# Kernel optimization log

Hardware: AMD Instinct MI355X
Metric: run time of the kernel (lower is better)

## Reference

```python
import jax, jax.numpy as jnp
import numpy as np

N_ATOMS = 262144          # 2**18 atoms
N_PAIRS = 16777216        # 2**24 pairs (~64 neighbors/atom)
SIGMA = 1.0
EPSILON = 1.0
CUTOFF = 2.5              # 2.5 * sigma (module default)


def setup_inputs() -> dict:
    key = jax.random.key(0)
    k_pos, k_i, k_off = jax.random.split(key, 3)
    # Gaussian cloud, scale 2 -> typical pair distances O(1-5), many inside cutoff
    positions = 2.0 * jax.random.normal(k_pos, (N_ATOMS, 3), dtype=jnp.float32)
    # Large box; shifts are zero so cell does not alter displacements
    cell = 100.0 * jnp.eye(3, dtype=jnp.float32)
    # Neighbor-list style pairs; guarantee j != i so distances are strictly > 0
    i = jax.random.randint(k_i, (N_PAIRS,), 0, N_ATOMS, dtype=jnp.int32)
    off = jax.random.randint(k_off, (N_PAIRS,), 1, N_ATOMS, dtype=jnp.int32)
    j = (i + off) % N_ATOMS
    mapping = jnp.stack([i, j])  # [2, n_pairs]
    shifts = jnp.zeros((N_PAIRS, 3), dtype=jnp.float32)
    return {"positions": positions, "cell": cell, "mapping": mapping, "shifts": shifts}


def reference(positions, cell, mapping, shifts):
    # Gather pair displacements: dr = r_j - r_i + shifts @ cell (row-vector cell)
    i, j = mapping[0], mapping[1]
    dr_vec = positions[j] - positions[i] + shifts @ cell      # [P, 3]
    distances = jnp.sqrt(jnp.sum(dr_vec * dr_vec, axis=-1))   # [P]

    # Lennard-Jones 12-6 pair energy: 4 eps ((s/r)^12 - (s/r)^6)
    sr6 = (SIGMA / distances) ** 6
    sr12 = sr6 * sr6
    pair_energies = 4.0 * EPSILON * (sr12 - sr6)
    mask = distances < CUTOFF
    pair_energies = jnp.where(mask, pair_energies, 0.0)
    energy = 0.5 * jnp.sum(pair_energies)

    # Pair force magnitude: 24 eps / r * (2 (s/r)^12 - (s/r)^6)
    pair_forces = 24.0 * EPSILON / distances * (2.0 * sr12 - sr6)
    pair_forces = jnp.where(mask, pair_forces, 0.0)
    force_vectors = (pair_forces / distances)[:, None] * dr_vec  # [P, 3]

    # Scatter-add back to atoms: -fv at i, +fv at j
    forces = (jnp.zeros_like(positions)
              .at[i].add(-force_vectors)
              .at[j].add(force_vectors))
    return energy, forces
```

## Files before the change

kernel.cpp:

```cpp
#include <hip/hip_runtime.h>

#define N_ATOMS 262144
#define N_PAIRS 16777216
#define FCOMP (N_ATOMS * 3)

#define NB      256
#define BSHIFT  10
#define ALOCAL  (N_ATOMS / NB)
#define CAPBB   32
#define SC_THREADS 256
#define NPT     32
#define PPB     (SC_THREADS * NPT)
#define G_TOTAL (N_PAIRS / PPB)
#define ACC_THREADS 1024

typedef int          v4i __attribute__((ext_vector_type(4)));
typedef float        v4f __attribute__((ext_vector_type(4)));
typedef unsigned int u32;
typedef u32          v4u __attribute__((ext_vector_type(4)));


__device__ __forceinline__ void atomic_add_f32(float* addr, float v) {
    unsafeAtomicAdd(addr, v);
}
__device__ __forceinline__ float scrub_nonfinite(float x) {
    return ((__float_as_uint(x) & 0x7f800000u) == 0x7f800000u) ? 0.0f : x;
}

__global__ void __launch_bounds__(256) lj_prep_kernel(
    const float* __restrict__ pos, v4f* __restrict__ pos4,
    float* __restrict__ forces, double* __restrict__ ews)
{
    const int a = blockIdx.x * blockDim.x + threadIdx.x;
    if (a < N_ATOMS) {
        v4f p = {pos[3 * a + 0], pos[3 * a + 1], pos[3 * a + 2], 0.0f};
        pos4[a] = p;
        forces[3 * a + 0] = 0.0f;
        forces[3 * a + 1] = 0.0f;
        forces[3 * a + 2] = 0.0f;
    }
    if (a == 0) *ews = 0.0;
}

__global__ void __launch_bounds__(SC_THREADS, 7) lj_scatter_kernel(
    const v4f* __restrict__ pos4,
    const float* __restrict__ cell,
    const int* __restrict__ map_i,
    const int* __restrict__ map_j,
    const float* __restrict__ shifts,
    v4u* __restrict__ records,
    u32* __restrict__ cnts,
    int pair_base, int g_count,
    double* __restrict__ energy_ws)
{
    __shared__ u32 hist[NB];
    __shared__ double wave_sums[SC_THREADS / 64];

    const int tid = threadIdx.x;
    const int g   = blockIdx.x;
    if (tid < NB) hist[tid] = 0;
    __syncthreads();

    const float c00 = cell[0], c01 = cell[1], c02 = cell[2];
    const float c10 = cell[3], c11 = cell[4], c12 = cell[5];
    const float c20 = cell[6], c21 = cell[7], c22 = cell[8];

    double e_acc = 0.0;
    const size_t rec_base = (size_t)g * NB * CAPBB;

    auto do_pair = [&](int i, int j, float sx, float sy, float sz) {
        const float shx = sx * c00 + sy * c10 + sz * c20;
        const float shy = sx * c01 + sy * c11 + sz * c21;
        const float shz = sx * c02 + sy * c12 + sz * c22;
        const v4f Pi = pos4[i];
        const v4f Pj = pos4[j];
        const float dx = Pj.x - Pi.x + shx;
        const float dy = Pj.y - Pi.y + shy;
        const float dz = Pj.z - Pi.z + shz;
        const float r2 = dx * dx + dy * dy + dz * dz;
        if (r2 < 6.25f) {
            const float inv_r2 = 1.0f / r2;
            const float sr6  = inv_r2 * inv_r2 * inv_r2;
            const float sr12 = sr6 * sr6;
            e_acc += (double)scrub_nonfinite(4.0f * (sr12 - sr6));
            const float pf = 24.0f * inv_r2 * (2.0f * sr12 - sr6);
            const float fx = scrub_nonfinite(pf * dx);
            const float fy = scrub_nonfinite(pf * dy);
            const float fz = scrub_nonfinite(pf * dz);
            const u32 bi = ((u32)i) >> BSHIFT;
            const u32 bj = ((u32)j) >> BSHIFT;
            const u32 si = atomicAdd(&hist[bi], 1u);
            if (si < CAPBB) {
                v4u ri = {(u32)i, __float_as_uint(-fx), __float_as_uint(-fy), __float_as_uint(-fz)};
                __builtin_nontemporal_store(ri, &records[rec_base + (size_t)bi * CAPBB + si]);
            }
            const u32 sj = atomicAdd(&hist[bj], 1u);
            if (sj < CAPBB) {
                v4u rj = {(u32)j, __float_as_uint(fx), __float_as_uint(fy), __float_as_uint(fz)};
                __builtin_nontemporal_store(rj, &records[rec_base + (size_t)bj * CAPBB + sj]);
            }
        }
    };

    const int base4 = pair_base / 4;
    #pragma unroll
    for (int s = 0; s < NPT / 4; ++s) {
        const int e = base4 + (s * g_count + g) * SC_THREADS + tid;
        const v4i mi = __builtin_nontemporal_load(((const v4i*)map_i) + e);
        const v4i mj = __builtin_nontemporal_load(((const v4i*)map_j) + e);
        const v4f sa = __builtin_nontemporal_load(((const v4f*)shifts) + 3 * e + 0);
        const v4f sb = __builtin_nontemporal_load(((const v4f*)shifts) + 3 * e + 1);
        const v4f sc = __builtin_nontemporal_load(((const v4f*)shifts) + 3 * e + 2);
        do_pair(mi.x, mj.x, sa.x, sa.y, sa.z);
        do_pair(mi.y, mj.y, sa.w, sb.x, sb.y);
        do_pair(mi.z, mj.z, sb.z, sb.w, sc.x);
        do_pair(mi.w, mj.w, sc.y, sc.z, sc.w);
    }
    __syncthreads();

    if (tid < NB) {
        const u32 c = hist[tid];
        cnts[(size_t)g * NB + tid] = (c < CAPBB) ? c : (u32)CAPBB;
    }

    for (int off = 32; off > 0; off >>= 1)
        e_acc += __shfl_down(e_acc, off, 64);
    const int lane = tid & 63, wid = tid >> 6;
    if (lane == 0) wave_sums[wid] = e_acc;
    __syncthreads();
    if (tid == 0) {
        double s = 0.0;
        for (int w = 0; w < SC_THREADS / 64; ++w) s += wave_sums[w];
        atomicAdd(energy_ws, s);
    }
}

__global__ void __launch_bounds__(ACC_THREADS) lj_accum_kernel(
    const v4u* __restrict__ records,
    const u32* __restrict__ cnts,
    int g_count,
    float* __restrict__ forces)
{
    __shared__ float facc[ALOCAL * 3];
    __shared__ u32 lcnt[G_TOTAL];
    const int b = blockIdx.x;
    const int tid = threadIdx.x;

    for (int t = tid; t < ALOCAL * 3; t += ACC_THREADS) facc[t] = 0.0f;
    for (int t = tid; t < g_count; t += ACC_THREADS) lcnt[t] = cnts[(size_t)t * NB + b];
    __syncthreads();

    const int total = g_count * CAPBB;
    for (int r = tid; r < total; r += ACC_THREADS) {
        const int g = r >> 5;
        const int k = r & (CAPBB - 1);
        if ((u32)k < lcnt[g]) {
            const v4u rec = records[((size_t)g * NB + b) * CAPBB + k];
            const u32 al = rec.x & (ALOCAL - 1);
            atomicAdd(&facc[al * 3 + 0], __uint_as_float(rec.y));
            atomicAdd(&facc[al * 3 + 1], __uint_as_float(rec.z));
            atomicAdd(&facc[al * 3 + 2], __uint_as_float(rec.w));
        }
    }
    __syncthreads();

    const int fbase = (b << BSHIFT) * 3;
    for (int t = tid; t < ALOCAL * 3; t += ACC_THREADS)
        forces[fbase + t] += facc[t];
}

__global__ void __launch_bounds__(256) lj_zero_kernel(float* __restrict__ buf, int n,
                                                      double* __restrict__ ews) {
    int idx = blockIdx.x * blockDim.x + threadIdx.x;
    int stride = gridDim.x * blockDim.x;
    for (int k = idx; k < n; k += stride) buf[k] = 0.0f;
    if (idx == 0) *ews = 0.0;
}

__global__ void __launch_bounds__(256) lj_pair_direct_kernel(
    const float* __restrict__ pos,
    const float* __restrict__ cell,
    const int* __restrict__ map_i,
    const int* __restrict__ map_j,
    const float* __restrict__ shifts,
    float* __restrict__ forces,
    double* __restrict__ energy_ws)
{
    const float c00 = cell[0], c01 = cell[1], c02 = cell[2];
    const float c10 = cell[3], c11 = cell[4], c12 = cell[5];
    const float c20 = cell[6], c21 = cell[7], c22 = cell[8];
    double e_acc = 0.0;
    const int t = blockIdx.x * blockDim.x + threadIdx.x;
    const v4i mi = ((const v4i*)map_i)[t];
    const v4i mj = ((const v4i*)map_j)[t];
    const v4f sa = ((const v4f*)shifts)[3 * t + 0];
    const v4f sb = ((const v4f*)shifts)[3 * t + 1];
    const v4f sc = ((const v4f*)shifts)[3 * t + 2];
    auto body = [&](int i, int j, float sx, float sy, float sz) {
        const float shx = sx * c00 + sy * c10 + sz * c20;
        const float shy = sx * c01 + sy * c11 + sz * c21;
        const float shz = sx * c02 + sy * c12 + sz * c22;
        const float dx = pos[3*j]   - pos[3*i]   + shx;
        const float dy = pos[3*j+1] - pos[3*i+1] + shy;
        const float dz = pos[3*j+2] - pos[3*i+2] + shz;
        const float r2 = dx*dx + dy*dy + dz*dz;
        if (r2 < 6.25f) {
            const float inv_r2 = 1.0f / r2;
            const float sr6 = inv_r2*inv_r2*inv_r2, sr12 = sr6*sr6;
            e_acc += (double)scrub_nonfinite(4.0f * (sr12 - sr6));
            const float pf = 24.0f * inv_r2 * (2.0f * sr12 - sr6);
            const float fx = scrub_nonfinite(pf*dx), fy = scrub_nonfinite(pf*dy), fz = scrub_nonfinite(pf*dz);
            atomic_add_f32(&forces[3*i+0], -fx); atomic_add_f32(&forces[3*i+1], -fy); atomic_add_f32(&forces[3*i+2], -fz);
            atomic_add_f32(&forces[3*j+0],  fx); atomic_add_f32(&forces[3*j+1],  fy); atomic_add_f32(&forces[3*j+2],  fz);
        }
    };
    body(mi.x, mj.x, sa.x, sa.y, sa.z);
    body(mi.y, mj.y, sa.w, sb.x, sb.y);
    body(mi.z, mj.z, sb.z, sb.w, sc.x);
    body(mi.w, mj.w, sc.y, sc.z, sc.w);
    for (int off = 32; off > 0; off >>= 1) e_acc += __shfl_down(e_acc, off, 64);
    __shared__ double ws4[4];
    if ((threadIdx.x & 63) == 0) ws4[threadIdx.x >> 6] = e_acc;
    __syncthreads();
    if (threadIdx.x == 0) atomicAdd(energy_ws, ws4[0] + ws4[1] + ws4[2] + ws4[3]);
}

__global__ void __launch_bounds__(256) lj_scrub_kernel(float* __restrict__ buf, int n) {
    int idx = blockIdx.x * blockDim.x + threadIdx.x;
    int stride = gridDim.x * blockDim.x;
    for (int k = idx; k < n; k += stride) buf[k] = scrub_nonfinite(buf[k]);
}

__global__ void lj_finalize_kernel(float* __restrict__ out, const double* __restrict__ ews) {
    out[0] = scrub_nonfinite((float)(0.5 * *ews));
}

extern "C" void kernel_launch(void* const* d_in, const int* in_sizes, int n_in,
                              void* d_out, int out_size, void* d_ws, size_t ws_size,
                              hipStream_t stream) {
    const float* positions = (const float*)d_in[0];
    const float* cell      = (const float*)d_in[1];
    const int*   map_i     = (const int*)d_in[2];
    const int*   map_j     = map_i + N_PAIRS;
    const float* shifts    = (const float*)d_in[3];

    float*  out    = (float*)d_out;
    float*  forces = out + 1;
    double* ews    = (double*)d_ws;
    v4f*    pos4   = (v4f*)((char*)d_ws + 64);

    int C = 0;
    {
        const int cands[6] = {1, 2, 4, 8, 16, 32};
        for (int ci = 0; ci < 6; ++ci) {
            const int c = cands[ci];
            const size_t gc = G_TOTAL / c;
            const size_t need = 64 + (size_t)N_ATOMS * 16
                              + gc * NB * 4
                              + gc * NB * CAPBB * 16;
            if (need <= ws_size) { C = c; break; }
        }
    }

    if (C > 0) {
        const int gc = G_TOTAL / C;
        const int pc = N_PAIRS / C;
        u32* cnts    = (u32*)((char*)d_ws + 64 + (size_t)N_ATOMS * 16);
        v4u* records = (v4u*)((char*)cnts + (size_t)gc * NB * 4);

        lj_prep_kernel<<<N_ATOMS / 256, 256, 0, stream>>>(positions, pos4, forces, ews);
        for (int c = 0; c < C; ++c) {
            lj_scatter_kernel<<<gc, SC_THREADS, 0, stream>>>(
                pos4, cell, map_i, map_j, shifts, records, cnts, c * pc, gc, ews);
            lj_accum_kernel<<<NB, ACC_THREADS, 0, stream>>>(records, cnts, gc, forces);
        }
        lj_scrub_kernel<<<1024, 256, 0, stream>>>(forces, FCOMP);
    } else {
        lj_zero_kernel<<<2048, 256, 0, stream>>>(forces, FCOMP, ews);
        lj_pair_direct_kernel<<<N_PAIRS / 4 / 256, 256, 0, stream>>>(
            positions, cell, map_i, map_j, shifts, forces, ews);
        lj_scrub_kernel<<<1024, 256, 0, stream>>>(forces, FCOMP);
    }
    lj_finalize_kernel<<<1, 1, 0, stream>>>(out, ews);
}
```

Measured before the change: 463.8 us.

## Software-pipeline index loads and position gathers across pair batches in scatter kernel

Restructures the scatter kernel's pair loop into a manual three-stage software pipeline: index/shift loads run two batches ahead and position gathers one batch ahead of the force computation. The aim is to hide gather latency with more memory-level parallelism per thread. To leave room for the extra live registers, the launch-bounds occupancy hint drops from 7 to 3 blocks per CU. Record stores also switch from nontemporal to normal stores, which may change how they are cached.

```diff
diff --git a/kernel.cpp b/kernel.cpp
--- a/kernel.cpp
+++ b/kernel.cpp
@@ -42,7 +42,7 @@
     if (a == 0) *ews = 0.0;
 }
 
-__global__ void __launch_bounds__(SC_THREADS, 7) lj_scatter_kernel(
+__global__ void __launch_bounds__(SC_THREADS, 3) lj_scatter_kernel(
     const v4f* __restrict__ pos4,
     const float* __restrict__ cell,
     const int* __restrict__ map_i,
@@ -67,13 +67,16 @@
 
     double e_acc = 0.0;
     const size_t rec_base = (size_t)g * NB * CAPBB;
-
-    auto do_pair = [&](int i, int j, float sx, float sy, float sz) {
+    const int base4 = pair_base / 4;
+    const v4i* mi4 = (const v4i*)map_i;
+    const v4i* mj4 = (const v4i*)map_j;
+    const v4f* sh4 = (const v4f*)shifts;
+
+    auto do_pair = [&](int i, int j, const v4f& Pi, const v4f& Pj,
+                       float sx, float sy, float sz) {
         const float shx = sx * c00 + sy * c10 + sz * c20;
         const float shy = sx * c01 + sy * c11 + sz * c21;
         const float shz = sx * c02 + sy * c12 + sz * c22;
-        const v4f Pi = pos4[i];
-        const v4f Pj = pos4[j];
         const float dx = Pj.x - Pi.x + shx;
         const float dy = Pj.y - Pi.y + shy;
         const float dz = Pj.z - Pi.z + shz;
@@ -92,30 +95,52 @@
             const u32 si = atomicAdd(&hist[bi], 1u);
             if (si < CAPBB) {
                 v4u ri = {(u32)i, __float_as_uint(-fx), __float_as_uint(-fy), __float_as_uint(-fz)};
-                __builtin_nontemporal_store(ri, &records[rec_base + (size_t)bi * CAPBB + si]);
+                records[rec_base + (size_t)bi * CAPBB + si] = ri;
             }
             const u32 sj = atomicAdd(&hist[bj], 1u);
             if (sj < CAPBB) {
                 v4u rj = {(u32)j, __float_as_uint(fx), __float_as_uint(fy), __float_as_uint(fz)};
-                __builtin_nontemporal_store(rj, &records[rec_base + (size_t)bj * CAPBB + sj]);
+                records[rec_base + (size_t)bj * CAPBB + sj] = rj;
             }
         }
     };
 
-    const int base4 = pair_base / 4;
-    #pragma unroll
-    for (int s = 0; s < NPT / 4; ++s) {
-        const int e = base4 + (s * g_count + g) * SC_THREADS + tid;
-        const v4i mi = __builtin_nontemporal_load(((const v4i*)map_i) + e);
-        const v4i mj = __builtin_nontemporal_load(((const v4i*)map_j) + e);
-        const v4f sa = __builtin_nontemporal_load(((const v4f*)shifts) + 3 * e + 0);
-        const v4f sb = __builtin_nontemporal_load(((const v4f*)shifts) + 3 * e + 1);
-        const v4f sc = __builtin_nontemporal_load(((const v4f*)shifts) + 3 * e + 2);
-        do_pair(mi.x, mj.x, sa.x, sa.y, sa.z);
-        do_pair(mi.y, mj.y, sa.w, sb.x, sb.y);
-        do_pair(mi.z, mj.z, sb.z, sb.w, sc.x);
-        do_pair(mi.w, mj.w, sc.y, sc.z, sc.w);
-    }
+#define S_IDX(S, s_) \
+    const int e##S = base4 + ((s_) * g_count + g) * SC_THREADS + tid; \
+    const v4i mi##S = __builtin_nontemporal_load(mi4 + e##S); \
+    const v4i mj##S = __builtin_nontemporal_load(mj4 + e##S); \
+    const v4f sa##S = __builtin_nontemporal_load(sh4 + 3 * e##S + 0); \
+    const v4f sb##S = __builtin_nontemporal_load(sh4 + 3 * e##S + 1); \
+    const v4f sc##S = __builtin_nontemporal_load(sh4 + 3 * e##S + 2);
+
+#define S_GATHER(S) \
+    const v4f Pi0##S = pos4[mi##S.x]; const v4f Pj0##S = pos4[mj##S.x]; \
+    const v4f Pi1##S = pos4[mi##S.y]; const v4f Pj1##S = pos4[mj##S.y]; \
+    const v4f Pi2##S = pos4[mi##S.z]; const v4f Pj2##S = pos4[mj##S.z]; \
+    const v4f Pi3##S = pos4[mi##S.w]; const v4f Pj3##S = pos4[mj##S.w];
+
+#define S_COMP(S) \
+    do_pair(mi##S.x, mj##S.x, Pi0##S, Pj0##S, sa##S.x, sa##S.y, sa##S.z); \
+    do_pair(mi##S.y, mj##S.y, Pi1##S, Pj1##S, sa##S.w, sb##S.x, sb##S.y); \
+    do_pair(mi##S.z, mj##S.z, Pi2##S, Pj2##S, sb##S.z, sb##S.w, sc##S.x); \
+    do_pair(mi##S.w, mj##S.w, Pi3##S, Pj3##S, sc##S.y, sc##S.z, sc##S.w);
+
+    S_IDX(A, 0)
+    S_IDX(B, 1)
+    S_GATHER(A)
+    S_IDX(C, 2)  S_GATHER(B)  S_COMP(A)
+    S_IDX(D, 3)  S_GATHER(C)  S_COMP(B)
+    S_IDX(E, 4)  S_GATHER(D)  S_COMP(C)
+    S_IDX(F, 5)  S_GATHER(E)  S_COMP(D)
+    S_IDX(G2, 6) S_GATHER(F)  S_COMP(E)
+    S_IDX(H, 7)  S_GATHER(G2) S_COMP(F)
+    S_GATHER(H)  S_COMP(G2)
+    S_COMP(H)
+
+#undef S_IDX
+#undef S_GATHER
+#undef S_COMP
+
     __syncthreads();
 
     if (tid < NB) {
```

After: 431.7 us. 6.9% less time.

## Software-pipeline position gathers via global_load_lds double buffering in scatter kernel

Applied to the files above, without the earlier changes.

Rewrites the scatter kernel's pair loop as a manually double-buffered pipeline. Position gathers for the next stage are issued directly into LDS with global_load_lds while the current stage is computed, and index/shift loads are prefetched one stage ahead. Block size drops to 128 threads, which doubles the record/count workspace per pair and adds a chunk count of 64 as a fallback. The accumulate kernel's record loads become nontemporal. The trade-off is full vmcnt(0) waits at every stage and a larger grid, in exchange for more memory-level parallelism on the random gathers.

```diff
diff --git a/kernel.cpp b/kernel.cpp
--- a/kernel.cpp
+++ b/kernel.cpp
@@ -8,17 +8,18 @@
 #define BSHIFT  10
 #define ALOCAL  (N_ATOMS / NB)
 #define CAPBB   32
-#define SC_THREADS 256
+#define SC_THREADS 128
 #define NPT     32
 #define PPB     (SC_THREADS * NPT)
 #define G_TOTAL (N_PAIRS / PPB)
+#define STG     4
+#define NSTG    (NPT / STG)
 #define ACC_THREADS 1024
 
 typedef int          v4i __attribute__((ext_vector_type(4)));
 typedef float        v4f __attribute__((ext_vector_type(4)));
 typedef unsigned int u32;
 typedef u32          v4u __attribute__((ext_vector_type(4)));
-
 
 __device__ __forceinline__ void atomic_add_f32(float* addr, float v) {
     unsafeAtomicAdd(addr, v);
@@ -42,7 +43,7 @@
     if (a == 0) *ews = 0.0;
 }
 
-__global__ void __launch_bounds__(SC_THREADS, 7) lj_scatter_kernel(
+__global__ void __launch_bounds__(SC_THREADS) lj_scatter_kernel(
     const v4f* __restrict__ pos4,
     const float* __restrict__ cell,
     const int* __restrict__ map_i,
@@ -53,12 +54,15 @@
     int pair_base, int g_count,
     double* __restrict__ energy_ws)
 {
+    __shared__ v4f stage_lds[2][SC_THREADS / 64][2 * STG][64];
     __shared__ u32 hist[NB];
     __shared__ double wave_sums[SC_THREADS / 64];
 
-    const int tid = threadIdx.x;
-    const int g   = blockIdx.x;
-    if (tid < NB) hist[tid] = 0;
+    const int tid  = threadIdx.x;
+    const int g    = blockIdx.x;
+    const int wid  = tid >> 6;
+    const int lane = tid & 63;
+    for (int t = tid; t < NB; t += SC_THREADS) hist[t] = 0;
     __syncthreads();
 
     const float c00 = cell[0], c01 = cell[1], c02 = cell[2];
@@ -67,13 +71,16 @@
 
     double e_acc = 0.0;
     const size_t rec_base = (size_t)g * NB * CAPBB;
-
-    auto do_pair = [&](int i, int j, float sx, float sy, float sz) {
+    const int base4 = pair_base / 4;
+    const v4i* mi4 = (const v4i*)map_i;
+    const v4i* mj4 = (const v4i*)map_j;
+    const v4f* sh4 = (const v4f*)shifts;
+
+    auto do_pair = [&](int i, int j, const v4f& Pi, const v4f& Pj,
+                       float sx, float sy, float sz) {
         const float shx = sx * c00 + sy * c10 + sz * c20;
         const float shy = sx * c01 + sy * c11 + sz * c21;
         const float shz = sx * c02 + sy * c12 + sz * c22;
-        const v4f Pi = pos4[i];
-        const v4f Pj = pos4[j];
         const float dx = Pj.x - Pi.x + shx;
         const float dy = Pj.y - Pi.y + shy;
         const float dz = Pj.z - Pi.z + shz;
@@ -102,30 +109,69 @@
         }
     };
 
-    const int base4 = pair_base / 4;
-    #pragma unroll
-    for (int s = 0; s < NPT / 4; ++s) {
-        const int e = base4 + (s * g_count + g) * SC_THREADS + tid;
-        const v4i mi = __builtin_nontemporal_load(((const v4i*)map_i) + e);
-        const v4i mj = __builtin_nontemporal_load(((const v4i*)map_j) + e);
-        const v4f sa = __builtin_nontemporal_load(((const v4f*)shifts) + 3 * e + 0);
-        const v4f sb = __builtin_nontemporal_load(((const v4f*)shifts) + 3 * e + 1);
-        const v4f sc = __builtin_nontemporal_load(((const v4f*)shifts) + 3 * e + 2);
-        do_pair(mi.x, mj.x, sa.x, sa.y, sa.z);
-        do_pair(mi.y, mj.y, sa.w, sb.x, sb.y);
-        do_pair(mi.z, mj.z, sb.z, sb.w, sc.x);
-        do_pair(mi.w, mj.w, sc.y, sc.z, sc.w);
-    }
-    __syncthreads();
-
-    if (tid < NB) {
-        const u32 c = hist[tid];
-        cnts[(size_t)g * NB + tid] = (c < CAPBB) ? c : (u32)CAPBB;
+#define VM0 asm volatile("s_waitcnt vmcnt(0)" ::: "memory"); \
+            __builtin_amdgcn_sched_barrier(0);
+
+#define IDX_DECL(S) v4i mi##S, mj##S; v4f sa##S, sb##S, sc##S;
+#define IDX_LOAD(S, t) { \
+    const int e_ = base4 + ((t) * g_count + g) * SC_THREADS + tid; \
+    mi##S = __builtin_nontemporal_load(mi4 + e_); \
+    mj##S = __builtin_nontemporal_load(mj4 + e_); \
+    sa##S = __builtin_nontemporal_load(sh4 + 3 * e_ + 0); \
+    sb##S = __builtin_nontemporal_load(sh4 + 3 * e_ + 1); \
+    sc##S = __builtin_nontemporal_load(sh4 + 3 * e_ + 2); }
+
+#define GLDS_ONE(d, slot, atom) \
+    __builtin_amdgcn_global_load_lds( \
+        (const __attribute__((address_space(1))) void*)(pos4 + (atom)), \
+        (__attribute__((address_space(3))) void*)(u32)(uintptr_t)(&stage_lds[d][wid][slot][0]), \
+        16, 0, 0);
+
+#define GLDS_STAGE(d, S) \
+    GLDS_ONE(d, 0, mi##S.x) GLDS_ONE(d, 1, mj##S.x) \
+    GLDS_ONE(d, 2, mi##S.y) GLDS_ONE(d, 3, mj##S.y) \
+    GLDS_ONE(d, 4, mi##S.z) GLDS_ONE(d, 5, mj##S.z) \
+    GLDS_ONE(d, 6, mi##S.w) GLDS_ONE(d, 7, mj##S.w)
+
+#define COMP_STAGE(d, S) { \
+    const v4f Pi0 = stage_lds[d][wid][0][lane]; const v4f Pj0 = stage_lds[d][wid][1][lane]; \
+    const v4f Pi1 = stage_lds[d][wid][2][lane]; const v4f Pj1 = stage_lds[d][wid][3][lane]; \
+    const v4f Pi2 = stage_lds[d][wid][4][lane]; const v4f Pj2 = stage_lds[d][wid][5][lane]; \
+    const v4f Pi3 = stage_lds[d][wid][6][lane]; const v4f Pj3 = stage_lds[d][wid][7][lane]; \
+    do_pair(mi##S.x, mj##S.x, Pi0, Pj0, sa##S.x, sa##S.y, sa##S.z); \
+    do_pair(mi##S.y, mj##S.y, Pi1, Pj1, sa##S.w, sb##S.x, sb##S.y); \
+    do_pair(mi##S.z, mj##S.z, Pi2, Pj2, sb##S.z, sb##S.w, sc##S.x); \
+    do_pair(mi##S.w, mj##S.w, Pi3, Pj3, sc##S.y, sc##S.z, sc##S.w); }
+
+    IDX_DECL(A) IDX_DECL(B)
+    IDX_LOAD(A, 0)
+    GLDS_STAGE(0, A)
+    IDX_LOAD(B, 1)
+    VM0 GLDS_STAGE(1, B) COMP_STAGE(0, A) IDX_LOAD(A, 2)
+    VM0 GLDS_STAGE(0, A) COMP_STAGE(1, B) IDX_LOAD(B, 3)
+    VM0 GLDS_STAGE(1, B) COMP_STAGE(0, A) IDX_LOAD(A, 4)
+    VM0 GLDS_STAGE(0, A) COMP_STAGE(1, B) IDX_LOAD(B, 5)
+    VM0 GLDS_STAGE(1, B) COMP_STAGE(0, A) IDX_LOAD(A, 6)
+    VM0 GLDS_STAGE(0, A) COMP_STAGE(1, B) IDX_LOAD(B, 7)
+    VM0 GLDS_STAGE(1, B) COMP_STAGE(0, A)
+    VM0 COMP_STAGE(1, B)
+
+#undef VM0
+#undef IDX_DECL
+#undef IDX_LOAD
+#undef GLDS_ONE
+#undef GLDS_STAGE
+#undef COMP_STAGE
+
+    __syncthreads();
+
+    for (int t = tid; t < NB; t += SC_THREADS) {
+        const u32 c = hist[t];
+        cnts[(size_t)g * NB + t] = (c < CAPBB) ? c : (u32)CAPBB;
     }
 
     for (int off = 32; off > 0; off >>= 1)
         e_acc += __shfl_down(e_acc, off, 64);
-    const int lane = tid & 63, wid = tid >> 6;
     if (lane == 0) wave_sums[wid] = e_acc;
     __syncthreads();
     if (tid == 0) {
@@ -155,7 +201,7 @@
         const int g = r >> 5;
         const int k = r & (CAPBB - 1);
         if ((u32)k < lcnt[g]) {
-            const v4u rec = records[((size_t)g * NB + b) * CAPBB + k];
+            const v4u rec = __builtin_nontemporal_load(&records[((size_t)g * NB + b) * CAPBB + k]);
             const u32 al = rec.x & (ALOCAL - 1);
             atomicAdd(&facc[al * 3 + 0], __uint_as_float(rec.y));
             atomicAdd(&facc[al * 3 + 1], __uint_as_float(rec.z));
@@ -251,8 +297,8 @@
 
     int C = 0;
     {
-        const int cands[6] = {1, 2, 4, 8, 16, 32};
-        for (int ci = 0; ci < 6; ++ci) {
+        const int cands[7] = {1, 2, 4, 8, 16, 32, 64};
+        for (int ci = 0; ci < 7; ++ci) {
             const int c = cands[ci];
             const size_t gc = G_TOTAL / c;
             const size_t need = 64 + (size_t)N_ATOMS * 16
```

Result: no change. 463.8 us (+0.0%).
